# Performance work log

Hardware: AMD Instinct MI355X
Metric: run time of the kernel (lower is better)

Reference implementation:

```python
import jax, jax.numpy as jnp
import numpy as np

CONNECTIVITY_WEIGHT = 1.0
HOLE_WEIGHT = 0.5
SUBSAMPLE = 128  # original strides sequences longer than 128
N_TRIPLETS = 32


def _pairwise_dist(x):
    # x: [B, Tc, D] -> Euclidean distance matrix [B, Tc, Tc] (torch.cdist p=2)
    sqn = jnp.sum(x * x, axis=-1)  # [B, Tc]
    sq = sqn[:, :, None] + sqn[:, None, :] - 2.0 * jnp.einsum('bid,bjd->bij', x, x)
    sq = jnp.maximum(sq, 0.0)
    # safe sqrt: zero gradient at zero distance (matches torch.cdist behavior)
    sq_safe = jnp.where(sq > 0, sq, 1.0)
    return jnp.where(sq > 0, jnp.sqrt(sq_safe), 0.0)


def setup_inputs() -> dict:
    key = jax.random.key(0)
    k1, k2 = jax.random.split(key)
    B, T, D = 128, 2048, 512
    latent_batch = jax.random.normal(k1, (B, T, D), dtype=jnp.float32)
    connection_threshold = jnp.ones((1,), dtype=jnp.float32)
    triplet_idx = jax.random.randint(k2, (B, N_TRIPLETS, 3), 0, SUBSAMPLE, dtype=jnp.int32)
    return {
        'latent_batch': latent_batch,
        'connection_threshold': connection_threshold,
        'triplet_idx': triplet_idx,
    }


def reference(latent_batch, connection_threshold, triplet_idx):
    B, T, D = latent_batch.shape
    stride = max(T // SUBSAMPLE, 1)
    x = latent_batch[:, ::stride, :]  # [B, Tc, D], static slice
    Tc = x.shape[1]

    d = _pairwise_dist(x)  # [B, Tc, Tc]

    threshold = jnp.abs(connection_threshold[0]) + 0.1
    # sigmoid(-(d - thr)) == sigmoid(thr - d)
    p = jax.nn.sigmoid(threshold - d)
    conn_sum = jnp.sum(p, axis=(1, 2)) - jnp.trace(p, axis1=1, axis2=2)  # [B]
    denom = Tc * (Tc - 1) + 1e-8
    connectivity_loss = 1.0 - conn_sum / denom  # [B]

    # random-triplet hole loss
    b_idx = jnp.arange(B)[:, None]
    i0, i1, i2 = triplet_idx[..., 0], triplet_idx[..., 1], triplet_idx[..., 2]
    d01 = d[b_idx, i0, i1]  # [B, N_TRIPLETS]
    d02 = d[b_idx, i0, i2]
    d12 = d[b_idx, i1, i2]
    edges = jnp.stack([d01, d02, d12], axis=-1)  # [B, N_TRIPLETS, 3]
    edge_var = jnp.var(edges, axis=-1, ddof=1)  # torch.var default unbiased
    hole_loss = jnp.mean(jnp.exp(-edge_var), axis=-1)  # [B]

    avg_loss = (CONNECTIVITY_WEIGHT * jnp.mean(connectivity_loss)
                + HOLE_WEIGHT * jnp.mean(hole_loss))
    return avg_loss
```

## Files before the change

kernel.cpp:

```cpp
#include <hip/hip_runtime.h>
#include <math.h>

#define NB 128
#define TC 128
#define DD 512
#define TSTR 16
#define KT 64
#define NT (DD/KT)
#define XP 72
#define DST 132
#define NTRIP 32

typedef __attribute__((ext_vector_type(8))) short bf16x8;
typedef __attribute__((ext_vector_type(8))) unsigned short u16x8;
typedef __attribute__((ext_vector_type(4))) float f32x4;

__device__ __forceinline__ unsigned short f2bf(float f) {
  unsigned int u = __float_as_uint(f);
  return (unsigned short)((u + 0x7fffu + ((u >> 16) & 1u)) >> 16);
}

__global__ __launch_bounds__(1024) void topo_fused(
    const float* __restrict__ latent,
    const float* __restrict__ thr,
    const int*   __restrict__ trip,
    float* __restrict__ partial)
{
  const int b    = blockIdx.x;
  const int tid  = threadIdx.x;
  const int lane = tid & 63;
  const int wid  = tid >> 6;
  const int wrow = (wid >> 2) * 32;
  const int wcol = (wid & 3) * 32;

  __shared__ __align__(16) unsigned short xt[2][TC][XP];
  __shared__ float dmat[TC][DST];
  __shared__ float sqn[TC];
  __shared__ float wred[16];

  const float* xb = latent + (size_t)b * (2048 * 512);

  const int srow = tid >> 3;
  const int skc  = (tid & 7) * 8;
  const float* sp = xb + (size_t)srow * (TSTR * DD) + skc;

  f32x4 acc[2][2];
#pragma unroll
  for (int i = 0; i < 2; ++i)
#pragma unroll
    for (int j = 0; j < 2; ++j)
#pragma unroll
      for (int r = 0; r < 4; ++r) acc[i][j][r] = 0.f;

  {
    float4 pa = *reinterpret_cast<const float4*>(sp);
    float4 pb = *reinterpret_cast<const float4*>(sp + 4);
    u16x8 w;
    w[0]=f2bf(pa.x); w[1]=f2bf(pa.y); w[2]=f2bf(pa.z); w[3]=f2bf(pa.w);
    w[4]=f2bf(pb.x); w[5]=f2bf(pb.y); w[6]=f2bf(pb.z); w[7]=f2bf(pb.w);
    *reinterpret_cast<u16x8*>(&xt[0][srow][skc]) = w;
  }

  const int r0  = wrow + (lane & 15);
  const int c0  = wcol + (lane & 15);
  const int kk0 = (lane >> 4) << 3;

  for (int t = 0; t < NT; ++t) {
    float4 pa, pb;
    const bool pf = (t + 1 < NT);
    if (pf) {
      pa = *reinterpret_cast<const float4*>(sp + (t + 1) * KT);
      pb = *reinterpret_cast<const float4*>(sp + (t + 1) * KT + 4);
    }
    __syncthreads();
    if (pf) {
      u16x8 w;
      w[0]=f2bf(pa.x); w[1]=f2bf(pa.y); w[2]=f2bf(pa.z); w[3]=f2bf(pa.w);
      w[4]=f2bf(pb.x); w[5]=f2bf(pb.y); w[6]=f2bf(pb.z); w[7]=f2bf(pb.w);
      *reinterpret_cast<u16x8*>(&xt[(t + 1) & 1][srow][skc]) = w;
    }
    const int cur = t & 1;
#pragma unroll
    for (int sub = 0; sub < 2; ++sub) {
      const int kk = sub * 32 + kk0;
      bf16x8 a0 = *reinterpret_cast<const bf16x8*>(&xt[cur][r0][kk]);
      bf16x8 a1 = *reinterpret_cast<const bf16x8*>(&xt[cur][r0 + 16][kk]);
      bf16x8 b0 = *reinterpret_cast<const bf16x8*>(&xt[cur][c0][kk]);
      bf16x8 b1 = *reinterpret_cast<const bf16x8*>(&xt[cur][c0 + 16][kk]);
      acc[0][0] = __builtin_amdgcn_mfma_f32_16x16x32_bf16(a0, b0, acc[0][0], 0, 0, 0);
      acc[0][1] = __builtin_amdgcn_mfma_f32_16x16x32_bf16(a0, b1, acc[0][1], 0, 0, 0);
      acc[1][0] = __builtin_amdgcn_mfma_f32_16x16x32_bf16(a1, b0, acc[1][0], 0, 0, 0);
      acc[1][1] = __builtin_amdgcn_mfma_f32_16x16x32_bf16(a1, b1, acc[1][1], 0, 0, 0);
    }
  }

  const int rbase = (lane >> 4) << 2;
  const int cidx  = lane & 15;
#pragma unroll
  for (int fr = 0; fr < 2; ++fr)
#pragma unroll
    for (int fc = 0; fc < 2; ++fc)
#pragma unroll
      for (int reg = 0; reg < 4; ++reg) {
        int grow = wrow + fr * 16 + rbase + reg;
        int gcol = wcol + fc * 16 + cidx;
        if (grow == gcol) sqn[grow] = acc[fr][fc][reg];
      }
  __syncthreads();

  const float thv = fabsf(thr[0]) + 0.1f;
  float psum = 0.f;
#pragma unroll
  for (int fr = 0; fr < 2; ++fr)
#pragma unroll
    for (int fc = 0; fc < 2; ++fc)
#pragma unroll
      for (int reg = 0; reg < 4; ++reg) {
        int grow = wrow + fr * 16 + rbase + reg;
        int gcol = wcol + fc * 16 + cidx;
        float g  = acc[fr][fc][reg];
        float sq = fmaxf(sqn[grow] + sqn[gcol] - 2.f * g, 0.f);
        float d  = sqrtf(sq);
        dmat[grow][gcol] = d;
        if (grow != gcol) psum += 1.f / (1.f + __expf(d - thv));
      }

#pragma unroll
  for (int off = 32; off; off >>= 1) psum += __shfl_down(psum, off, 64);
  if (lane == 0) wred[wid] = psum;
  __syncthreads();

  if (wid == 0) {
    float h = 0.f;
    if (lane < NTRIP) {
      const int* tp = trip + ((size_t)b * NTRIP + lane) * 3;
      int i0 = tp[0], i1 = tp[1], i2 = tp[2];
      float e0 = dmat[i0][i1], e1 = dmat[i0][i2], e2 = dmat[i1][i2];
      float m  = (e0 + e1 + e2) * (1.f / 3.f);
      float d0 = e0 - m, d1 = e1 - m, d2 = e2 - m;
      float v  = (d0 * d0 + d1 * d1 + d2 * d2) * 0.5f;
      h = __expf(-v);
    }
#pragma unroll
    for (int off = 32; off; off >>= 1) h += __shfl_down(h, off, 64);
    if (lane == 0) {
      float conn = 0.f;
#pragma unroll
      for (int w = 0; w < 16; ++w) conn += wred[w];
      partial[b]      = 1.f - conn / 16256.0f;
      partial[NB + b] = h * (1.f / NTRIP);
    }
  }
}

__global__ void topo_final(const float* __restrict__ partial, float* __restrict__ out)
{
  const int t = threadIdx.x;
  float v = partial[t] + 0.5f * partial[NB + t];
#pragma unroll
  for (int off = 32; off; off >>= 1) v += __shfl_down(v, off, 64);
  __shared__ float s2[2];
  if ((t & 63) == 0) s2[t >> 6] = v;
  __syncthreads();
  if (t == 0) out[0] = (s2[0] + s2[1]) * (1.f / NB);
}

extern "C" void kernel_launch(void* const* d_in, const int* in_sizes, int n_in,
                              void* d_out, int out_size, void* d_ws, size_t ws_size,
                              hipStream_t stream) {
  const float* latent = (const float*)d_in[0];
  const float* thr    = (const float*)d_in[1];
  const int*   trip   = (const int*)d_in[2];
  float* partial = (float*)d_ws;

  topo_fused<<<NB, 1024, 0, stream>>>(latent, thr, trip, partial);
  topo_final<<<1, 128, 0, stream>>>(partial, (float*)d_out);
}
```

Baseline: 18.73 us.

## Issue all global loads upfront and stage bf16 tiles from registers

Each thread now issues all eight of its global float4 load pairs at kernel start instead of one k-tile per iteration. The first half is converted to bf16 immediately and the second half at iteration three, so later LDS writes come from registers and the loop no longer waits on global latency. The barrier moves to the end of each iteration. This raises register pressure at 1024 threads per block and adds a barrier before the loop.

After: 19.49 us. 4.1% more time.

```diff
diff --git a/kernel.cpp b/kernel.cpp
--- a/kernel.cpp
+++ b/kernel.cpp
@@ -18,6 +18,13 @@
 __device__ __forceinline__ unsigned short f2bf(float f) {
   unsigned int u = __float_as_uint(f);
   return (unsigned short)((u + 0x7fffu + ((u >> 16) & 1u)) >> 16);
+}
+
+__device__ __forceinline__ u16x8 cvt8(float4 a, float4 b) {
+  u16x8 w;
+  w[0]=f2bf(a.x); w[1]=f2bf(a.y); w[2]=f2bf(a.z); w[3]=f2bf(a.w);
+  w[4]=f2bf(b.x); w[5]=f2bf(b.y); w[6]=f2bf(b.z); w[7]=f2bf(b.w);
+  return w;
 }
 
 __global__ __launch_bounds__(1024) void topo_fused(
@@ -44,6 +51,22 @@
   const int skc  = (tid & 7) * 8;
   const float* sp = xb + (size_t)srow * (TSTR * DD) + skc;
 
+  float4 pA[4][2], pB[4][2];
+#pragma unroll
+  for (int t = 0; t < 4; ++t) {
+    pA[t][0] = *reinterpret_cast<const float4*>(sp + t * KT);
+    pA[t][1] = *reinterpret_cast<const float4*>(sp + t * KT + 4);
+  }
+#pragma unroll
+  for (int t = 0; t < 4; ++t) {
+    pB[t][0] = *reinterpret_cast<const float4*>(sp + (t + 4) * KT);
+    pB[t][1] = *reinterpret_cast<const float4*>(sp + (t + 4) * KT + 4);
+  }
+
+  u16x8 rb[8];
+#pragma unroll
+  for (int t = 0; t < 4; ++t) rb[t] = cvt8(pA[t][0], pA[t][1]);
+
   f32x4 acc[2][2];
 #pragma unroll
   for (int i = 0; i < 2; ++i)
@@ -52,33 +75,20 @@
 #pragma unroll
       for (int r = 0; r < 4; ++r) acc[i][j][r] = 0.f;
 
-  {
-    float4 pa = *reinterpret_cast<const float4*>(sp);
-    float4 pb = *reinterpret_cast<const float4*>(sp + 4);
-    u16x8 w;
-    w[0]=f2bf(pa.x); w[1]=f2bf(pa.y); w[2]=f2bf(pa.z); w[3]=f2bf(pa.w);
-    w[4]=f2bf(pb.x); w[5]=f2bf(pb.y); w[6]=f2bf(pb.z); w[7]=f2bf(pb.w);
-    *reinterpret_cast<u16x8*>(&xt[0][srow][skc]) = w;
-  }
-
   const int r0  = wrow + (lane & 15);
   const int c0  = wcol + (lane & 15);
   const int kk0 = (lane >> 4) << 3;
 
+  *reinterpret_cast<u16x8*>(&xt[0][srow][skc]) = rb[0];
+  __syncthreads();
+
   for (int t = 0; t < NT; ++t) {
-    float4 pa, pb;
-    const bool pf = (t + 1 < NT);
-    if (pf) {
-      pa = *reinterpret_cast<const float4*>(sp + (t + 1) * KT);
-      pb = *reinterpret_cast<const float4*>(sp + (t + 1) * KT + 4);
+    if (t == 3) {
+#pragma unroll
+      for (int q = 0; q < 4; ++q) rb[4 + q] = cvt8(pB[q][0], pB[q][1]);
     }
-    __syncthreads();
-    if (pf) {
-      u16x8 w;
-      w[0]=f2bf(pa.x); w[1]=f2bf(pa.y); w[2]=f2bf(pa.z); w[3]=f2bf(pa.w);
-      w[4]=f2bf(pb.x); w[5]=f2bf(pb.y); w[6]=f2bf(pb.z); w[7]=f2bf(pb.w);
-      *reinterpret_cast<u16x8*>(&xt[(t + 1) & 1][srow][skc]) = w;
-    }
+    if (t + 1 < NT)
+      *reinterpret_cast<u16x8*>(&xt[(t + 1) & 1][srow][skc]) = rb[t + 1];
     const int cur = t & 1;
 #pragma unroll
     for (int sub = 0; sub < 2; ++sub) {
@@ -92,6 +102,7 @@
       acc[1][0] = __builtin_amdgcn_mfma_f32_16x16x32_bf16(a1, b0, acc[1][0], 0, 0, 0);
       acc[1][1] = __builtin_amdgcn_mfma_f32_16x16x32_bf16(a1, b1, acc[1][1], 0, 0, 0);
     }
+    __syncthreads();
   }
 
   const int rbase = (lane >> 4) << 2;
```
